# Optimization experiments

Hardware: AMD Instinct MI355X
Metric: run time of the kernel (lower is better)

## Reference

```python
import jax, jax.numpy as jnp
import numpy as np

# TFMBSLinear forward: quantize input and weight to ternary {-1,0,1} via sign,
# compute out = sign(x) @ sign(W)^T (what the ternary fabric T-GEMV kernel
# computes, with zero-skip), then add float bias. The base-3 byte packing is a
# transport encoding only; the math is the ternary matmul.

def setup_inputs() -> dict:
    key = jax.random.key(0)
    k1, k2, k3 = jax.random.split(key, 3)
    B, IN, OUT = 8192, 2048, 2048
    x = jax.random.normal(k1, (B, IN), dtype=jnp.float32)
    # kaiming-uniform-ish init; only sign matters for the fabric kernel
    weight = jax.random.normal(k2, (OUT, IN), dtype=jnp.float32)
    fan_in_bound = 1.0 / np.sqrt(IN)
    bias = jax.random.uniform(k3, (OUT,), dtype=jnp.float32,
                              minval=-fan_in_bound, maxval=fan_in_bound)
    return {"input": x, "weight": weight, "bias": bias}

def reference(input, weight, bias):
    x_t = jnp.sign(input)    # ternary activations [B, IN]
    w_t = jnp.sign(weight)   # ternary weights     [OUT, IN]
    out = jnp.einsum('bi,oi->bo', x_t, w_t)  # T-GEMV accumulation, fp32
    return out + bias
```

## Files before the change

kernel.cpp:

```cpp
#include <hip/hip_runtime.h>


typedef int   intx4    __attribute__((ext_vector_type(4)));
typedef int   intx8    __attribute__((ext_vector_type(8)));
typedef float floatx16 __attribute__((ext_vector_type(16)));

static constexpr int M = 8192;
static constexpr int N = 2048;
static constexpr int K = 2048;
static constexpr int KB = K / 2;
static constexpr int BM = 256, BN = 256;

__device__ __forceinline__ unsigned nib(float v) {
    unsigned u = __float_as_uint(v);
    return (v != 0.0f) ? (0x2u | ((u >> 28) & 0x8u)) : 0u;
}

__device__ __forceinline__ unsigned pack8(const float4& a, const float4& b) {
    return  nib(a.x)        | (nib(a.y) << 4)  | (nib(a.z) << 8)  | (nib(a.w) << 12)
         | (nib(b.x) << 16) | (nib(b.y) << 20) | (nib(b.z) << 24) | (nib(b.w) << 28);
}

__global__ __launch_bounds__(256) void quant_tile(
    const float* __restrict__ x, const float* __restrict__ w,
    uint4* __restrict__ qx, uint4* __restrict__ qw, int nx, int ntot)
{
    int g = blockIdx.x * 256 + threadIdx.x;
    if (g >= ntot) return;
    const float* src; uint4* dst; int gg;
    if (g < nx) { gg = g; src = x; dst = qx; }
    else        { gg = g - nx; src = w; dst = qw; }
    const int r = gg & 31, h = (gg >> 5) & 1, c = (gg >> 6) & 31, s = gg >> 11;
    const int m = s * 32 + r;
    const float4* p = (const float4*)(src + (size_t)m * K + (c * 2 + h) * 32);
    uint4 o;
    o.x = pack8(p[0], p[1]);
    o.y = pack8(p[2], p[3]);
    o.z = pack8(p[4], p[5]);
    o.w = pack8(p[6], p[7]);
    dst[gg] = o;
}

__device__ __forceinline__ intx8 ext4(intx4 v) {
    return __builtin_shufflevector(v, v, 0, 1, 2, 3, -1, -1, -1, -1);
}

#define MFMA_(A_, B_, C_) __builtin_amdgcn_mfma_scale_f32_32x32x64_f8f6f4( \
    ext4(A_), ext4(B_), C_, 4, 4, 0, 127, 0, 127)

#define GLDS(g_, l_) __builtin_amdgcn_global_load_lds(                      \
    (const __attribute__((address_space(1))) void*)(g_),                    \
    (__attribute__((address_space(3))) void*)(l_), 16, 0, 0)

#define MFMA8()                               \
    acc[0][0] = MFMA_(a0, b0, acc[0][0]);     \
    acc[0][1] = MFMA_(a0, b1, acc[0][1]);     \
    acc[1][0] = MFMA_(a1, b0, acc[1][0]);     \
    acc[1][1] = MFMA_(a1, b1, acc[1][1]);     \
    acc[2][0] = MFMA_(a2, b0, acc[2][0]);     \
    acc[2][1] = MFMA_(a2, b1, acc[2][1]);     \
    acc[3][0] = MFMA_(a3, b0, acc[3][0]);     \
    acc[3][1] = MFMA_(a3, b1, acc[3][1])

#define FRAGS(FO)                                         \
    intx4 a0 = *(const intx4*)(fA + (FO));                \
    intx4 a1 = *(const intx4*)(fA + (FO) + 4096);         \
    intx4 a2 = *(const intx4*)(fA + (FO) + 8192);         \
    intx4 a3 = *(const intx4*)(fA + (FO) + 12288);        \
    intx4 b0 = *(const intx4*)(fB + (FO));                \
    intx4 b1 = *(const intx4*)(fB + (FO) + 4096)

__global__ __launch_bounds__(512, 2) void tgemm_fp4_256(
    const char* __restrict__ A,
    const char* __restrict__ B,
    const float* __restrict__ bias,
    float* __restrict__ C)
{
    __shared__ char smem[131072];

    const int tid  = threadIdx.x;
    const int wave = tid >> 6;
    const int lane = tid & 63;
    const int l32  = lane & 31;
    const int half = lane >> 5;
    const int wm2  = wave >> 2;
    const int wn4  = wave & 3;

    const int bi   = blockIdx.x;
    const int slot = bi >> 3;
    const int bm   = ((bi & 7) * 4 + (slot >> 3)) * 256;
    const int bn   = (slot & 7) * 256;

    const char* gA = A + ((size_t)(bm >> 5) + wave) * 32768 + lane * 16;
    const char* gB = B + ((size_t)(bn >> 5) + wave) * 32768 + lane * 16;
    char* stA = smem + wave * 4096;
    char* stB = smem + 65536 + wave * 4096;

    const char* fA = smem + (wm2 * 4) * 4096 + lane * 16;
    const char* fB = smem + 65536 + (wn4 * 2) * 4096 + lane * 16;

    floatx16 acc[4][2] = {};

    #pragma unroll
    for (int c = 0; c < 4; ++c) {
        GLDS(gA + c * 1024, stA + c * 1024);
        GLDS(gB + c * 1024, stB + c * 1024);
    }
    asm volatile("s_waitcnt vmcnt(6)" ::: "memory");
    __builtin_amdgcn_s_barrier();

    for (int t = 0; t < 7; ++t) {
        const int buf  = (t & 1) * 32768;
        const int xbuf = buf ^ 32768;
        const char* ga = gA + (size_t)(t + 1) * 4096;
        const char* gb = gB + (size_t)(t + 1) * 4096;
        #pragma unroll
        for (int c = 0; c < 4; ++c) {
            FRAGS(buf + c * 1024);
            GLDS(ga + c * 1024, stA + xbuf + c * 1024);
            GLDS(gb + c * 1024, stB + xbuf + c * 1024);
            asm volatile("s_waitcnt vmcnt(6)" ::: "memory");
            __builtin_amdgcn_s_barrier();
            __builtin_amdgcn_s_setprio(1);
            MFMA8();
            __builtin_amdgcn_s_setprio(0);
            __builtin_amdgcn_s_barrier();
        }
    }

    {
        const int buf = 32768;
        #pragma unroll
        for (int c = 0; c < 4; ++c) {
            FRAGS(buf + c * 1024);
            if (c == 0) { asm volatile("s_waitcnt vmcnt(4)" ::: "memory"); __builtin_amdgcn_s_barrier(); }
            if (c == 1) { asm volatile("s_waitcnt vmcnt(2)" ::: "memory"); __builtin_amdgcn_s_barrier(); }
            if (c == 2) { asm volatile("s_waitcnt vmcnt(0)" ::: "memory"); __builtin_amdgcn_s_barrier(); }
            __builtin_amdgcn_s_setprio(1);
            MFMA8();
            __builtin_amdgcn_s_setprio(0);
            if (c < 3) __builtin_amdgcn_s_barrier();
        }
    }

    const int cn0 = bn + wn4 * 64 + l32;
    const float bc0 = bias[cn0];
    const float bc1 = bias[cn0 + 32];
    const int rbase = bm + wm2 * 128 + 4 * half;

    #pragma unroll
    for (int i = 0; i < 4; ++i) {
        #pragma unroll
        for (int r = 0; r < 16; ++r) {
            const int row = rbase + 32 * i + (r & 3) + 8 * (r >> 2);
            C[(size_t)row * N + cn0]      = acc[i][0][r] + bc0;
            C[(size_t)row * N + cn0 + 32] = acc[i][1][r] + bc1;
        }
    }
}

extern "C" void kernel_launch(void* const* d_in, const int* in_sizes, int n_in,
                              void* d_out, int out_size, void* d_ws, size_t ws_size,
                              hipStream_t stream) {
    const float* x    = (const float*)d_in[0];
    const float* w    = (const float*)d_in[1];
    const float* bias = (const float*)d_in[2];
    float* out = (float*)d_out;

    char* qx = (char*)d_ws;
    char* qw = qx + (size_t)M * KB;

    const int nx   = (M * KB) / 16;
    const int ntot = nx + (N * KB) / 16;
    quant_tile<<<ntot / 256, 256, 0, stream>>>(
        x, w, (uint4*)qx, (uint4*)qw, nx, ntot);

    tgemm_fp4_256<<<dim3((M / BM) * (N / BN)), dim3(512), 0, stream>>>(
        qx, qw, bias, out);
}
```

Measured before the change: 142.6 us.

## Shrink GEMM tile to 256x128 with 4 waves and finer-grained K pipeline

Replaces the 256x256, 8-wave, 128KB-LDS block with a 256x128, 4-wave block using 48KB of LDS. The K loop now runs in 128-wide stages of two 64-wide chunks, and one barrier per chunk replaces two. The grid doubles to 512 blocks and the block-to-tile swizzle is remapped. Smaller LDS per block should allow more resident blocks and better latency hiding, at the cost of less reuse of the A tile and more global traffic for A.

```diff
diff --git a/kernel.cpp b/kernel.cpp
--- a/kernel.cpp
+++ b/kernel.cpp
@@ -9,7 +9,7 @@
 static constexpr int N = 2048;
 static constexpr int K = 2048;
 static constexpr int KB = K / 2;
-static constexpr int BM = 256, BN = 256;
+static constexpr int BM = 256, BN = 128;
 
 __device__ __forceinline__ unsigned nib(float v) {
     unsigned u = __float_as_uint(v);
@@ -62,91 +62,96 @@
     acc[3][0] = MFMA_(a3, b0, acc[3][0]);     \
     acc[3][1] = MFMA_(a3, b1, acc[3][1])
 
-#define FRAGS(FO)                                         \
-    intx4 a0 = *(const intx4*)(fA + (FO));                \
-    intx4 a1 = *(const intx4*)(fA + (FO) + 4096);         \
-    intx4 a2 = *(const intx4*)(fA + (FO) + 8192);         \
-    intx4 a3 = *(const intx4*)(fA + (FO) + 12288);        \
-    intx4 b0 = *(const intx4*)(fB + (FO));                \
-    intx4 b1 = *(const intx4*)(fB + (FO) + 4096)
+#define FRAGS(BUF_, C_)                                                     \
+    intx4 a0 = *(const intx4*)(smem + (BUF_) + fAo          + (C_) * 1024); \
+    intx4 a1 = *(const intx4*)(smem + (BUF_) + fAo + 2048   + (C_) * 1024); \
+    intx4 a2 = *(const intx4*)(smem + (BUF_) + fAo + 4096   + (C_) * 1024); \
+    intx4 a3 = *(const intx4*)(smem + (BUF_) + fAo + 6144   + (C_) * 1024); \
+    intx4 b0 = *(const intx4*)(smem + (BUF_) + fBo          + (C_) * 1024); \
+    intx4 b1 = *(const intx4*)(smem + (BUF_) + fBo + 2048   + (C_) * 1024)
 
-__global__ __launch_bounds__(512, 2) void tgemm_fp4_256(
+__global__ __launch_bounds__(256, 2) void tgemm_fp4_256x128(
     const char* __restrict__ A,
     const char* __restrict__ B,
     const float* __restrict__ bias,
     float* __restrict__ C)
 {
-    __shared__ char smem[131072];
+    __shared__ char smem[49152];
 
     const int tid  = threadIdx.x;
     const int wave = tid >> 6;
     const int lane = tid & 63;
     const int l32  = lane & 31;
     const int half = lane >> 5;
-    const int wm2  = wave >> 2;
-    const int wn4  = wave & 3;
 
-    const int bi   = blockIdx.x;
-    const int slot = bi >> 3;
-    const int bm   = ((bi & 7) * 4 + (slot >> 3)) * 256;
-    const int bn   = (slot & 7) * 256;
+    const int bi    = blockIdx.x;
+    const int local = bi >> 3;
+    const int bm    = ((bi & 7) * 4 + (local & 3)) * 256;
+    const int bn    = (local >> 2) * 128;
 
-    const char* gA = A + ((size_t)(bm >> 5) + wave) * 32768 + lane * 16;
-    const char* gB = B + ((size_t)(bn >> 5) + wave) * 32768 + lane * 16;
-    char* stA = smem + wave * 4096;
-    char* stB = smem + 65536 + wave * 4096;
+    const char* gA0 = A + ((size_t)(bm >> 5) + 2 * wave) * 32768 + lane * 16;
+    const char* gA1 = gA0 + 32768;
+    const char* gB0 = B + ((size_t)(bn >> 5) + wave) * 32768 + lane * 16;
+    const int stA0 = (2 * wave) * 2048;
+    const int stA1 = stA0 + 2048;
+    const int stB0 = 16384 + wave * 2048;
 
-    const char* fA = smem + (wm2 * 4) * 4096 + lane * 16;
-    const char* fB = smem + 65536 + (wn4 * 2) * 4096 + lane * 16;
+    const int wm = (wave & 1) * 128;
+    const int wn = (wave >> 1) * 64;
+    const int fAo = (wm >> 5) * 2048 + lane * 16;
+    const int fBo = 16384 + (wn >> 5) * 2048 + lane * 16;
 
     floatx16 acc[4][2] = {};
 
     #pragma unroll
-    for (int c = 0; c < 4; ++c) {
-        GLDS(gA + c * 1024, stA + c * 1024);
-        GLDS(gB + c * 1024, stB + c * 1024);
+    for (int c = 0; c < 2; ++c) {
+        GLDS(gA0 + c * 1024, smem + stA0 + c * 1024);
+        GLDS(gA1 + c * 1024, smem + stA1 + c * 1024);
+        GLDS(gB0 + c * 1024, smem + stB0 + c * 1024);
     }
-    asm volatile("s_waitcnt vmcnt(6)" ::: "memory");
-    __builtin_amdgcn_s_barrier();
 
-    for (int t = 0; t < 7; ++t) {
-        const int buf  = (t & 1) * 32768;
-        const int xbuf = buf ^ 32768;
-        const char* ga = gA + (size_t)(t + 1) * 4096;
-        const char* gb = gB + (size_t)(t + 1) * 4096;
+    #pragma unroll
+    for (int t = 0; t < 15; ++t) {
+        const int buf  = (t & 1) * 24576;
+        const int xbuf = buf ^ 24576;
         #pragma unroll
-        for (int c = 0; c < 4; ++c) {
-            FRAGS(buf + c * 1024);
-            GLDS(ga + c * 1024, stA + xbuf + c * 1024);
-            GLDS(gb + c * 1024, stB + xbuf + c * 1024);
-            asm volatile("s_waitcnt vmcnt(6)" ::: "memory");
+        for (int c = 0; c < 2; ++c) {
+            asm volatile("s_waitcnt vmcnt(3)" ::: "memory");
             __builtin_amdgcn_s_barrier();
+            FRAGS(buf, c);
+            const int g = (t + 1) * 2 + c;
+            GLDS(gA0 + g * 1024, smem + xbuf + stA0 + c * 1024);
+            GLDS(gA1 + g * 1024, smem + xbuf + stA1 + c * 1024);
+            GLDS(gB0 + g * 1024, smem + xbuf + stB0 + c * 1024);
             __builtin_amdgcn_s_setprio(1);
             MFMA8();
             __builtin_amdgcn_s_setprio(0);
-            __builtin_amdgcn_s_barrier();
         }
     }
 
     {
-        const int buf = 32768;
-        #pragma unroll
-        for (int c = 0; c < 4; ++c) {
-            FRAGS(buf + c * 1024);
-            if (c == 0) { asm volatile("s_waitcnt vmcnt(4)" ::: "memory"); __builtin_amdgcn_s_barrier(); }
-            if (c == 1) { asm volatile("s_waitcnt vmcnt(2)" ::: "memory"); __builtin_amdgcn_s_barrier(); }
-            if (c == 2) { asm volatile("s_waitcnt vmcnt(0)" ::: "memory"); __builtin_amdgcn_s_barrier(); }
+        {
+            asm volatile("s_waitcnt vmcnt(3)" ::: "memory");
+            __builtin_amdgcn_s_barrier();
+            FRAGS(24576, 0);
             __builtin_amdgcn_s_setprio(1);
             MFMA8();
             __builtin_amdgcn_s_setprio(0);
-            if (c < 3) __builtin_amdgcn_s_barrier();
+        }
+        {
+            asm volatile("s_waitcnt vmcnt(0)" ::: "memory");
+            __builtin_amdgcn_s_barrier();
+            FRAGS(24576, 1);
+            __builtin_amdgcn_s_setprio(1);
+            MFMA8();
+            __builtin_amdgcn_s_setprio(0);
         }
     }
 
-    const int cn0 = bn + wn4 * 64 + l32;
+    const int cn0 = bn + wn + l32;
     const float bc0 = bias[cn0];
     const float bc1 = bias[cn0 + 32];
-    const int rbase = bm + wm2 * 128 + 4 * half;
+    const int rbase = bm + wm + 4 * half;
 
     #pragma unroll
     for (int i = 0; i < 4; ++i) {
@@ -175,6 +180,6 @@
     quant_tile<<<ntot / 256, 256, 0, stream>>>(
         x, w, (uint4*)qx, (uint4*)qw, nx, ntot);
 
-    tgemm_fp4_256<<<dim3((M / BM) * (N / BN)), dim3(512), 0, stream>>>(
+    tgemm_fp4_256x128<<<dim3((M / BM) * (N / BN)), dim3(256), 0, stream>>>(
         qx, qw, bias, out);
 }
```

Result: no change. 141.0 us, median of 2 (-1.1%).
